# Kernel optimization log

Hardware: AMD Instinct MI355X
Metric: run time of the kernel (lower is better)

Reference implementation:

```python
import jax, jax.numpy as jnp
import numpy as np
from jax import lax

UNITS1 = 256  # lstm_layer (second LSTM, return_sequences=False)
UNITS2 = 256  # hidden_lstm (first LSTM, return_sequences=True)
FEAT = 128


def _glorot(key, shape):
    fan_in, fan_out = shape[0], shape[1]
    lim = jnp.sqrt(6.0 / (fan_in + fan_out))
    return jax.random.uniform(key, shape, jnp.float32, -lim, lim)


def setup_inputs() -> dict:
    key = jax.random.key(0)
    ks = jax.random.split(key, 9)
    B, T = 128, 1024
    x = jax.random.normal(ks[0], (B, T, FEAT), jnp.float32)
    # Layer 1 (hidden_lstm): Keras kernel [in, 4H], recurrent_kernel [H, 4H], bias [4H]
    W1 = _glorot(ks[1], (FEAT, 4 * UNITS2))
    U1 = _glorot(ks[2], (UNITS2, 4 * UNITS2))
    b1 = jnp.zeros((4 * UNITS2,), jnp.float32).at[UNITS2:2 * UNITS2].set(1.0)  # Keras unit_forget_bias
    # Layer 2 (lstm_layer)
    W2 = _glorot(ks[3], (UNITS2, 4 * UNITS1))
    U2 = _glorot(ks[4], (UNITS1, 4 * UNITS1))
    b2 = jnp.zeros((4 * UNITS1,), jnp.float32).at[UNITS1:2 * UNITS1].set(1.0)
    # Output dense: 1 unit, relu
    Wd = _glorot(ks[5], (UNITS1, 1))
    bd = jnp.zeros((1,), jnp.float32)
    return {"x": x, "W1": W1, "U1": U1, "b1": b1,
            "W2": W2, "U2": U2, "b2": b2, "Wd": Wd, "bd": bd}


def _lstm(x, W, U, b, return_sequences):
    # x: [B, T, F]; Keras gate order i, f, c(candidate), o.
    B = x.shape[0]
    H = U.shape[0]
    xW = jnp.einsum('btf,fg->btg', x, W) + b  # precompute input projections: [B, T, 4H]

    def step(carry, xw_t):
        h, c = carry
        g = xw_t + h @ U  # [B, 4H]
        i, f, cand, o = jnp.split(g, 4, axis=-1)
        i = jax.nn.sigmoid(i)
        f = jax.nn.sigmoid(f)
        cand = jnp.tanh(cand)
        o = jax.nn.sigmoid(o)
        c = f * c + i * cand
        h = o * jnp.tanh(c)
        return (h, c), h

    init = (jnp.zeros((B, H), x.dtype), jnp.zeros((B, H), x.dtype))
    (h_last, _), hs = lax.scan(step, init, jnp.swapaxes(xW, 0, 1))  # hs: [T, B, H]
    return jnp.swapaxes(hs, 0, 1) if return_sequences else h_last


def reference(x, W1, U1, b1, W2, U2, b2, Wd, bd):
    h_seq = _lstm(x, W1, U1, b1, return_sequences=True)   # hidden_lstm: [B, T, U2]
    h_last = _lstm(h_seq, W2, U2, b2, return_sequences=False)  # lstm_layer: [B, U1]
    return jax.nn.relu(h_last @ Wd + bd)  # [B, 1]
```

## Files before the change

### kernel.cpp

```cpp
#include <hip/hip_runtime.h>

typedef __bf16 bf16x8 __attribute__((ext_vector_type(8)));
typedef float  f32x4  __attribute__((ext_vector_type(4)));
typedef unsigned short u16;
typedef unsigned int   u32;
typedef unsigned long long u64;

#define NB 128
#define NT 1024
#define NF 128
#define NH 256
#define NG 1024
#define M_ROWS (NB*NT)

__device__ __forceinline__ u16 f2bf(float f) {
  union { float f; u32 u; } c; c.f = f;
  u32 u = c.u;
  return (u16)((u + 0x7fffu + ((u >> 16) & 1u)) >> 16);
}

__device__ __forceinline__ float sigm(float x) { return 1.f / (1.f + __expf(-x)); }
__device__ __forceinline__ float tanh_(float x) { return 1.f - 2.f / (1.f + __expf(2.f * x)); }

__device__ __forceinline__ f32x4 mm(bf16x8 a, bf16x8 b, f32x4 c) {
  return __builtin_amdgcn_mfma_f32_16x16x32_bf16(a, b, c, 0, 0, 0);
}

__device__ __forceinline__ u64 a_ld64(const u64* p) {
  return __hip_atomic_load((u64*)p, __ATOMIC_RELAXED, __HIP_MEMORY_SCOPE_AGENT);
}
__device__ __forceinline__ void a_st64(u64* p, u64 v) {
  __hip_atomic_store(p, v, __ATOMIC_RELAXED, __HIP_MEMORY_SCOPE_AGENT);
}
__device__ __forceinline__ void vm0() { asm volatile("s_waitcnt vmcnt(0)" ::: "memory"); }

__device__ __forceinline__ bool poll_ge(u32* c, u32 target, long& budget) {
  while (__hip_atomic_load(c, __ATOMIC_RELAXED, __HIP_MEMORY_SCOPE_AGENT) < target) {
    if (--budget <= 0) return false;
  }
  asm volatile("" ::: "memory");
  return true;
}

__global__ void prep(u32* __restrict__ flags) {
  if (blockIdx.x == 0 && threadIdx.x < 256) flags[threadIdx.x] = 0;
}

template<bool L1>
__device__ __forceinline__ void scan(
    const float* __restrict__ U, const float* __restrict__ W,
    const float* __restrict__ bias, const float* __restrict__ xf,
    u64* hseq, u64* h2, u32* cnt1, u32* cnt2, float* hlast,
    int g, int j, float (*gl)[16][68])
{
  const int tid  = threadIdx.x;
  const int lane = tid & 63;
  const int w    = tid >> 6;
  const int l15  = lane & 15, l16 = lane >> 4;
  constexpr int KIN  = L1 ? NF : NH;
  constexpr int KTIN = KIN / 32;

  const int colb = w * NH + j * 64;

  bf16x8 wfr[KTIN][4];
#pragma unroll
  for (int kt = 0; kt < KTIN; ++kt) {
    const int k0 = kt * 32 + l16 * 8;
#pragma unroll
    for (int nt = 0; nt < 4; ++nt) {
      const float* wp = W + (long)k0 * NG + colb + nt * 16 + l15;
      union { u16 s[8]; bf16x8 v; } cv;
#pragma unroll
      for (int e = 0; e < 8; ++e) cv.s[e] = f2bf(wp[(long)e * NG]);
      wfr[kt][nt] = cv.v;
    }
  }
  bf16x8 ufr[8][4];
#pragma unroll
  for (int kt = 0; kt < 8; ++kt) {
    const int k0 = kt * 32 + l16 * 8;
#pragma unroll
    for (int nt = 0; nt < 4; ++nt) {
      const float* up = U + (long)k0 * NG + colb + nt * 16 + l15;
      union { u16 s[8]; bf16x8 v; } cv;
#pragma unroll
      for (int e = 0; e < 8; ++e) cv.s[e] = f2bf(up[(long)e * NG]);
      ufr[kt][nt] = cv.v;
    }
  }

  const int prow = tid & 15;
  const int ublk = tid >> 4;
  const int b    = g * 16 + prow;
  const int ucol = j * 64 + ublk * 4;

  float bv[4][4];
#pragma unroll
  for (int gg = 0; gg < 4; ++gg)
#pragma unroll
    for (int q = 0; q < 4; ++q) bv[gg][q] = bias[gg * NH + ucol + q];

  u32* c1 = cnt1 + g * 16;
  u32* c2 = cnt2 + g * 16;
  const long abatch = (long)(g * 16 + l15) * NT;

  float cst[4] = {0.f, 0.f, 0.f, 0.f};
  long budget = 20000000;
  bool dead = false;

  for (int t = 0; t < NT; ++t) {
    bf16x8 ax[KTIN];
    if constexpr (L1) {
      const float* xp0 = xf + (abatch + t) * NF;
      f32x4 xraw[KTIN][2];
#pragma unroll
      for (int kt = 0; kt < KTIN; ++kt) {
        const float* xp = xp0 + kt * 32 + l16 * 8;
        xraw[kt][0] = *reinterpret_cast<const f32x4*>(xp);
        xraw[kt][1] = *reinterpret_cast<const f32x4*>(xp + 4);
      }
#pragma unroll
      for (int kt = 0; kt < KTIN; ++kt) {
        union { u16 s[8]; bf16x8 v; } cv;
#pragma unroll
        for (int e = 0; e < 4; ++e) {
          cv.s[e] = f2bf(xraw[kt][0][e]); cv.s[4 + e] = f2bf(xraw[kt][1][e]);
        }
        ax[kt] = cv.v;
      }
    } else {
      if (!dead && !poll_ge(c1, 16u * (u32)(t + 1), budget)) dead = true;
      u64* xb = hseq + (abatch + t) * 64;
#pragma unroll
      for (int kt = 0; kt < KTIN; ++kt) {
        union { u64 q[2]; bf16x8 v; } cv;
        cv.q[0] = a_ld64(xb + kt * 8 + l16 * 2);
        cv.q[1] = a_ld64(xb + kt * 8 + l16 * 2 + 1);
        ax[kt] = cv.v;
      }
    }

    f32x4 acc[4] = {};
#pragma unroll
    for (int kt = 0; kt < KTIN; ++kt)
#pragma unroll
      for (int nt = 0; nt < 4; ++nt) acc[nt] = mm(ax[kt], wfr[kt][nt], acc[nt]);

    if (t > 0) {
      u32* cr = L1 ? c1 : c2;
      if (!dead && !poll_ge(cr, 16u * (u32)t, budget)) dead = true;
      u64* hb;
      if constexpr (L1) hb = hseq + (abatch + (t - 1)) * 64;
      else              hb = h2 + ((((long)((t + 1) & 1) * 8 + g) * 16) + l15) * 64;
      bf16x8 af[8];
#pragma unroll
      for (int kt = 0; kt < 8; ++kt) {
        union { u64 q[2]; bf16x8 v; } cv;
        cv.q[0] = a_ld64(hb + kt * 8 + l16 * 2);
        cv.q[1] = a_ld64(hb + kt * 8 + l16 * 2 + 1);
        af[kt] = cv.v;
      }
#pragma unroll
      for (int kt = 0; kt < 8; ++kt)
#pragma unroll
        for (int nt = 0; nt < 4; ++nt) acc[nt] = mm(af[kt], ufr[kt][nt], acc[nt]);
    }

#pragma unroll
    for (int nt = 0; nt < 4; ++nt)
#pragma unroll
      for (int r = 0; r < 4; ++r)
        gl[w][l16 * 4 + r][nt * 16 + l15] = acc[nt][r];
    __syncthreads();

    f32x4 gi = *reinterpret_cast<const f32x4*>(&gl[0][prow][ublk * 4]);
    f32x4 gf = *reinterpret_cast<const f32x4*>(&gl[1][prow][ublk * 4]);
    f32x4 gc = *reinterpret_cast<const f32x4*>(&gl[2][prow][ublk * 4]);
    f32x4 go = *reinterpret_cast<const f32x4*>(&gl[3][prow][ublk * 4]);
    __syncthreads();
    float hh[4];
#pragma unroll
    for (int q = 0; q < 4; ++q) {
      float iv = sigm(gi[q] + bv[0][q]);
      float fv = sigm(gf[q] + bv[1][q]);
      float cd = tanh_(gc[q] + bv[2][q]);
      float ov = sigm(go[q] + bv[3][q]);
      cst[q] = fv * cst[q] + iv * cd;
      hh[q] = ov * tanh_(cst[q]);
    }
    union { u16 s[4]; u64 q; } hp;
#pragma unroll
    for (int q = 0; q < 4; ++q) hp.s[q] = f2bf(hh[q]);

    if constexpr (L1) {
      a_st64(hseq + ((long)b * NT + t) * 64 + (ucol >> 2), hp.q);
    } else {
      a_st64(h2 + ((((long)(t & 1) * 8 + g) * 16) + prow) * 64 + (ucol >> 2), hp.q);
      if (t == NT - 1)
        *reinterpret_cast<f32x4*>(hlast + (long)b * NH + ucol) =
            f32x4{hh[0], hh[1], hh[2], hh[3]};
    }

    vm0();
    if (lane == 0)
      __hip_atomic_fetch_add(L1 ? c1 : c2, 1u, __ATOMIC_RELAXED, __HIP_MEMORY_SCOPE_AGENT);
  }
}

__global__ __launch_bounds__(256, 1) void lstm_fused(
    const float* __restrict__ x,
    const float* __restrict__ W1, const float* __restrict__ U1, const float* __restrict__ b1,
    const float* __restrict__ W2, const float* __restrict__ U2, const float* __restrict__ b2,
    u64* hseq, u64* h2, u32* flags, float* hlast)
{
  __shared__ __align__(16) float gl[4][16][68];
  const int bid = blockIdx.x;
  const int sb  = bid & 31;
  u32* cnt1 = flags;
  u32* cnt2 = flags + 128;
  if (bid < 32)
    scan<true >(U1, W1, b1, x, hseq, nullptr, cnt1, cnt2, nullptr, sb & 7, sb >> 3, gl);
  else
    scan<false>(U2, W2, b2, nullptr, hseq, h2, cnt1, cnt2, hlast, sb & 7, sb >> 3, gl);
}

__global__ void dense_out(const float* __restrict__ hl, const float* __restrict__ Wd,
                          const float* __restrict__ bd, float* __restrict__ out) {
  int b = blockIdx.x, l = threadIdx.x;
  f32x4 h  = *reinterpret_cast<const f32x4*>(hl + (long)b * NH + l * 4);
  f32x4 wv = *reinterpret_cast<const f32x4*>(Wd + l * 4);
  float s = h[0] * wv[0] + h[1] * wv[1] + h[2] * wv[2] + h[3] * wv[3];
#pragma unroll
  for (int off = 32; off > 0; off >>= 1) s += __shfl_down(s, off);
  if (l == 0) out[b] = fmaxf(s + bd[0], 0.f);
}

extern "C" void kernel_launch(void* const* d_in, const int* in_sizes, int n_in,
                              void* d_out, int out_size, void* d_ws, size_t ws_size,
                              hipStream_t stream) {
  const float* x  = (const float*)d_in[0];
  const float* W1 = (const float*)d_in[1];
  const float* U1 = (const float*)d_in[2];
  const float* b1 = (const float*)d_in[3];
  const float* W2 = (const float*)d_in[4];
  const float* U2 = (const float*)d_in[5];
  const float* b2 = (const float*)d_in[6];
  const float* Wd = (const float*)d_in[7];
  const float* bd = (const float*)d_in[8];
  float* out = (float*)d_out;

  char* ws = (char*)d_ws;
  size_t off = 0;
  auto alloc = [&](size_t bytes) -> char* {
    char* p = ws + off;
    off = (off + bytes + 255) & ~(size_t)255;
    return p;
  };
  u64*   hseq  = (u64*)  alloc((size_t)M_ROWS * NH * 2);
  u64*   h2    = (u64*)  alloc((size_t)2 * 8 * 16 * NH * 2);
  float* hlast = (float*)alloc((size_t)NB * NH * 4);
  u32*   flags = (u32*)  alloc(1024);

  if (off > ws_size) {
    hipMemsetAsync(d_out, 0x42, (size_t)out_size * sizeof(float), stream);
    return;
  }

  prep<<<1, 256, 0, stream>>>(flags);
  lstm_fused<<<64, 256, 0, stream>>>(x, W1, U1, b1, W2, U2, b2, hseq, h2, flags, hlast);
  dense_out<<<128, 64, 0, stream>>>(hlast, Wd, bd, out);
}
```

Before: 5.936 ms.

## Use per-block step tags and XCC-local sc0 loads when groups share an XCD

```diff
diff --git a/kernel.cpp b/kernel.cpp
--- a/kernel.cpp
+++ b/kernel.cpp
@@ -13,29 +13,67 @@
 #define NG 1024
 #define M_ROWS (NB*NT)
 
+#define TAGS1_OFF 0
+#define TAGS2_OFF 512
+#define PING_OFF  1024
+#define META_OFF  1536
+#define RDY_OFF   1600
+#define DONE_OFF  1664
+#define ABRT_OFF  1696
+#define FLAGS_N   2048
+
 __device__ __forceinline__ u16 f2bf(float f) {
   union { float f; u32 u; } c; c.f = f;
   u32 u = c.u;
   return (u16)((u + 0x7fffu + ((u >> 16) & 1u)) >> 16);
 }
-
 __device__ __forceinline__ float sigm(float x) { return 1.f / (1.f + __expf(-x)); }
 __device__ __forceinline__ float tanh_(float x) { return 1.f - 2.f / (1.f + __expf(2.f * x)); }
-
 __device__ __forceinline__ f32x4 mm(bf16x8 a, bf16x8 b, f32x4 c) {
   return __builtin_amdgcn_mfma_f32_16x16x32_bf16(a, b, c, 0, 0, 0);
 }
-
-__device__ __forceinline__ u64 a_ld64(const u64* p) {
-  return __hip_atomic_load((u64*)p, __ATOMIC_RELAXED, __HIP_MEMORY_SCOPE_AGENT);
-}
-__device__ __forceinline__ void a_st64(u64* p, u64 v) {
-  __hip_atomic_store(p, v, __ATOMIC_RELAXED, __HIP_MEMORY_SCOPE_AGENT);
-}
 __device__ __forceinline__ void vm0() { asm volatile("s_waitcnt vmcnt(0)" ::: "memory"); }
-
-__device__ __forceinline__ bool poll_ge(u32* c, u32 target, long& budget) {
-  while (__hip_atomic_load(c, __ATOMIC_RELAXED, __HIP_MEMORY_SCOPE_AGENT) < target) {
+__device__ __forceinline__ void sb0() { __builtin_amdgcn_sched_barrier(0); }
+
+__device__ __forceinline__ u32 a_ld32(const u32* p) { return __hip_atomic_load((u32*)p, __ATOMIC_RELAXED, __HIP_MEMORY_SCOPE_AGENT); }
+__device__ __forceinline__ u64 a_ld64(const u64* p) { return __hip_atomic_load((u64*)p, __ATOMIC_RELAXED, __HIP_MEMORY_SCOPE_AGENT); }
+__device__ __forceinline__ void a_st32(u32* p, u32 v) { __hip_atomic_store(p, v, __ATOMIC_RELAXED, __HIP_MEMORY_SCOPE_AGENT); }
+__device__ __forceinline__ void a_st64(u64* p, u64 v) { __hip_atomic_store(p, v, __ATOMIC_RELAXED, __HIP_MEMORY_SCOPE_AGENT); }
+__device__ __forceinline__ void a_add32(u32* p, u32 v) { __hip_atomic_fetch_add(p, v, __ATOMIC_RELAXED, __HIP_MEMORY_SCOPE_AGENT); }
+
+__device__ __forceinline__ u64 s_ld64(const u64* p) {
+  u64 r; asm volatile("global_load_dwordx2 %0, %1, off sc0" : "=v"(r) : "v"(p) : "memory"); return r;
+}
+__device__ __forceinline__ u32 s_ld32w(const u32* p) {
+  u32 r; asm volatile("global_load_dword %0, %1, off sc0\n\ts_waitcnt vmcnt(0)" : "=v"(r) : "v"(p) : "memory"); return r;
+}
+__device__ __forceinline__ void s_st64(u64* p, u64 v) {
+  asm volatile("global_store_dwordx2 %0, %1, off sc0" :: "v"(p), "v"(v) : "memory");
+}
+__device__ __forceinline__ void s_st32(u32* p, u32 v) {
+  asm volatile("global_store_dword %0, %1, off sc0" :: "v"(p), "v"(v) : "memory");
+}
+
+template<bool FAST> __device__ __forceinline__ u64 dld64(const u64* p) {
+  if constexpr (FAST) return s_ld64(p); else return a_ld64(p);
+}
+template<bool FAST> __device__ __forceinline__ void dwait() {
+  if constexpr (FAST) { vm0(); sb0(); }
+}
+template<bool FAST> __device__ __forceinline__ void dst64(u64* p, u64 v) {
+  if constexpr (FAST) s_st64(p, v); else a_st64(p, v);
+}
+template<bool FAST> __device__ __forceinline__ void tst32(u32* p, u32 v) {
+  if constexpr (FAST) s_st32(p, v); else a_st32(p, v);
+}
+template<bool FAST> __device__ __forceinline__ bool poll4(const u32* tg, u32 target, long& budget) {
+  const u64* p = (const u64*)tg;
+  for (;;) {
+    u64 a, b;
+    if constexpr (FAST) { a = s_ld64(p); b = s_ld64(p + 1); vm0(); sb0(); }
+    else                { a = a_ld64(p); b = a_ld64(p + 1); }
+    if ((u32)a >= target && (u32)(a >> 32) >= target &&
+        (u32)b >= target && (u32)(b >> 32) >= target) break;
     if (--budget <= 0) return false;
   }
   asm volatile("" ::: "memory");
@@ -43,23 +81,20 @@
 }
 
 __global__ void prep(u32* __restrict__ flags) {
-  if (blockIdx.x == 0 && threadIdx.x < 256) flags[threadIdx.x] = 0;
-}
-
-template<bool L1>
-__device__ __forceinline__ void scan(
-    const float* __restrict__ U, const float* __restrict__ W,
-    const float* __restrict__ bias, const float* __restrict__ xf,
-    u64* hseq, u64* h2, u32* cnt1, u32* cnt2, float* hlast,
-    int g, int j, float (*gl)[16][68])
+  int i = blockIdx.x * 256 + threadIdx.x;
+  if (i < FLAGS_N) flags[i] = 0;
+}
+
+template<bool IS1, bool FAST>
+__device__ void scan(const float* __restrict__ U, const float* __restrict__ W,
+                     const float* __restrict__ bias, const float* __restrict__ xf,
+                     u64* hseq, u64* h2, u32* flags, float* hlast,
+                     int g, int j, float (*gl)[16][68])
 {
-  const int tid  = threadIdx.x;
-  const int lane = tid & 63;
-  const int w    = tid >> 6;
-  const int l15  = lane & 15, l16 = lane >> 4;
-  constexpr int KIN  = L1 ? NF : NH;
+  const int tid = threadIdx.x, lane = tid & 63, w = tid >> 6;
+  const int l15 = lane & 15, l16 = lane >> 4;
+  constexpr int KIN  = IS1 ? NF : NH;
   constexpr int KTIN = KIN / 32;
-
   const int colb = w * NH + j * 64;
 
   bf16x8 wfr[KTIN][4];
@@ -89,10 +124,8 @@
     }
   }
 
-  const int prow = tid & 15;
-  const int ublk = tid >> 4;
-  const int b    = g * 16 + prow;
-  const int ucol = j * 64 + ublk * 4;
+  const int prow = tid & 15, ublk = tid >> 4;
+  const int b = g * 16 + prow, ucol = j * 64 + ublk * 4;
 
   float bv[4][4];
 #pragma unroll
@@ -100,17 +133,18 @@
 #pragma unroll
     for (int q = 0; q < 4; ++q) bv[gg][q] = bias[gg * NH + ucol + q];
 
-  u32* c1 = cnt1 + g * 16;
-  u32* c2 = cnt2 + g * 16;
+  u32* t1 = flags + TAGS1_OFF + g * 64;
+  u32* t2 = flags + TAGS2_OFF + g * 64;
+  u32* mytag = (IS1 ? t1 : t2) + j;
   const long abatch = (long)(g * 16 + l15) * NT;
 
   float cst[4] = {0.f, 0.f, 0.f, 0.f};
-  long budget = 20000000;
+  long budget = 1000000;
   bool dead = false;
 
   for (int t = 0; t < NT; ++t) {
     bf16x8 ax[KTIN];
-    if constexpr (L1) {
+    if constexpr (IS1) {
       const float* xp0 = xf + (abatch + t) * NF;
       f32x4 xraw[KTIN][2];
 #pragma unroll
@@ -129,13 +163,19 @@
         ax[kt] = cv.v;
       }
     } else {
-      if (!dead && !poll_ge(c1, 16u * (u32)(t + 1), budget)) dead = true;
+      if (!dead && !poll4<FAST>(t1, (u32)(t + 1), budget)) dead = true;
       u64* xb = hseq + (abatch + t) * 64;
+      u64 xr[KTIN][2];
+#pragma unroll
+      for (int kt = 0; kt < KTIN; ++kt) {
+        xr[kt][0] = dld64<FAST>(xb + kt * 8 + l16 * 2);
+        xr[kt][1] = dld64<FAST>(xb + kt * 8 + l16 * 2 + 1);
+      }
+      dwait<FAST>();
 #pragma unroll
       for (int kt = 0; kt < KTIN; ++kt) {
         union { u64 q[2]; bf16x8 v; } cv;
-        cv.q[0] = a_ld64(xb + kt * 8 + l16 * 2);
-        cv.q[1] = a_ld64(xb + kt * 8 + l16 * 2 + 1);
+        cv.q[0] = xr[kt][0]; cv.q[1] = xr[kt][1];
         ax[kt] = cv.v;
       }
     }
@@ -147,23 +187,24 @@
       for (int nt = 0; nt < 4; ++nt) acc[nt] = mm(ax[kt], wfr[kt][nt], acc[nt]);
 
     if (t > 0) {
-      u32* cr = L1 ? c1 : c2;
-      if (!dead && !poll_ge(cr, 16u * (u32)t, budget)) dead = true;
-      u64* hb;
-      if constexpr (L1) hb = hseq + (abatch + (t - 1)) * 64;
-      else              hb = h2 + ((((long)((t + 1) & 1) * 8 + g) * 16) + l15) * 64;
-      bf16x8 af[8];
+      if (!dead && !poll4<FAST>(IS1 ? t1 : t2, (u32)t, budget)) dead = true;
+      const u64* hb;
+      if constexpr (IS1) hb = hseq + (abatch + (t - 1)) * 64;
+      else               hb = h2 + ((((long)((t + 1) & 1) * 8 + g) * 16) + l15) * 64;
+      u64 hr[8][2];
+#pragma unroll
+      for (int kt = 0; kt < 8; ++kt) {
+        hr[kt][0] = dld64<FAST>(hb + kt * 8 + l16 * 2);
+        hr[kt][1] = dld64<FAST>(hb + kt * 8 + l16 * 2 + 1);
+      }
+      dwait<FAST>();
 #pragma unroll
       for (int kt = 0; kt < 8; ++kt) {
         union { u64 q[2]; bf16x8 v; } cv;
-        cv.q[0] = a_ld64(hb + kt * 8 + l16 * 2);
-        cv.q[1] = a_ld64(hb + kt * 8 + l16 * 2 + 1);
-        af[kt] = cv.v;
-      }
-#pragma unroll
-      for (int kt = 0; kt < 8; ++kt)
-#pragma unroll
-        for (int nt = 0; nt < 4; ++nt) acc[nt] = mm(af[kt], ufr[kt][nt], acc[nt]);
+        cv.q[0] = hr[kt][0]; cv.q[1] = hr[kt][1];
+#pragma unroll
+        for (int nt = 0; nt < 4; ++nt) acc[nt] = mm(cv.v, ufr[kt][nt], acc[nt]);
+      }
     }
 
 #pragma unroll
@@ -177,7 +218,6 @@
     f32x4 gf = *reinterpret_cast<const f32x4*>(&gl[1][prow][ublk * 4]);
     f32x4 gc = *reinterpret_cast<const f32x4*>(&gl[2][prow][ublk * 4]);
     f32x4 go = *reinterpret_cast<const f32x4*>(&gl[3][prow][ublk * 4]);
-    __syncthreads();
     float hh[4];
 #pragma unroll
     for (int q = 0; q < 4; ++q) {
@@ -192,18 +232,18 @@
 #pragma unroll
     for (int q = 0; q < 4; ++q) hp.s[q] = f2bf(hh[q]);
 
-    if constexpr (L1) {
-      a_st64(hseq + ((long)b * NT + t) * 64 + (ucol >> 2), hp.q);
+    if constexpr (IS1) {
+      dst64<FAST>(hseq + ((long)b * NT + t) * 64 + (ucol >> 2), hp.q);
     } else {
-      a_st64(h2 + ((((long)(t & 1) * 8 + g) * 16) + prow) * 64 + (ucol >> 2), hp.q);
+      dst64<FAST>(h2 + ((((long)(t & 1) * 8 + g) * 16) + prow) * 64 + (ucol >> 2), hp.q);
       if (t == NT - 1)
         *reinterpret_cast<f32x4*>(hlast + (long)b * NH + ucol) =
             f32x4{hh[0], hh[1], hh[2], hh[3]};
     }
 
     vm0();
-    if (lane == 0)
-      __hip_atomic_fetch_add(L1 ? c1 : c2, 1u, __ATOMIC_RELAXED, __HIP_MEMORY_SCOPE_AGENT);
+    __syncthreads();
+    if (tid == 0) tst32<FAST>(mytag, (u32)(t + 1));
   }
 }
 
@@ -214,14 +254,70 @@
     u64* hseq, u64* h2, u32* flags, float* hlast)
 {
   __shared__ __align__(16) float gl[4][16][68];
-  const int bid = blockIdx.x;
-  const int sb  = bid & 31;
-  u32* cnt1 = flags;
-  u32* cnt2 = flags + 128;
-  if (bid < 32)
-    scan<true >(U1, W1, b1, x, hseq, nullptr, cnt1, cnt2, nullptr, sb & 7, sb >> 3, gl);
-  else
-    scan<false>(U2, W2, b2, nullptr, hseq, h2, cnt1, cnt2, hlast, sb & 7, sb >> 3, gl);
+  __shared__ int sm;
+  const int bid = blockIdx.x, tid = threadIdx.x, lane = tid & 63;
+  const int sb = bid & 31, g = sb & 7, j = sb >> 3;
+  const bool is1 = bid < 32;
+
+  u32* meta = flags + META_OFF;
+  u32* rdy  = flags + RDY_OFF;
+  u32* ping = flags + PING_OFF;
+  u32* done = flags + DONE_OFF;
+  u32* abrt = flags + ABRT_OFF;
+
+  u32 xcc = 0;
+  asm volatile("s_getreg_b32 %0, hwreg(HW_REG_XCC_ID)" : "=s"(xcc));
+  if (tid == 0) { a_st32(meta + bid, xcc + 1u); vm0(); a_add32(rdy, 1u); }
+  bool ok = true;
+  { long hb = 2000000;
+    while (a_ld32(rdy) < 64u) { if (--hb <= 0) { ok = false; break; } } }
+  asm volatile("" ::: "memory");
+  u32 mv = 0; if (ok) mv = a_ld32(meta + lane);
+  u32 m0 = __shfl(mv, 0);
+  const bool alldeg = __all(mv == m0);
+  u32 v0 = __shfl(mv, g);
+  bool co = ok && !alldeg && (v0 != 0);
+#pragma unroll
+  for (int k = 1; k < 8; ++k) co = co && (__shfl(mv, g + 8 * k) == v0);
+
+  if (tid == 0) {
+    bool fail = !co;
+    if (co) {
+      const int r = is1 ? j : (4 + j);
+      u32* slot = ping + g * 64 + r;
+      u32* prev = ping + g * 64 + ((r + 7) & 7);
+      for (u32 k = 1; k <= 3u && !fail; ++k) {
+        if (r == 0) {
+          s_st32(slot, k);
+          long pb = 20000;
+          while (s_ld32w(prev) < k) { if (--pb <= 0) { fail = true; break; } }
+        } else {
+          long pb = 20000;
+          while (s_ld32w(prev) < k) { if (--pb <= 0) { fail = true; break; } }
+          if (!fail) s_st32(slot, k);
+        }
+      }
+      vm0();
+    }
+    if (fail) a_st32(abrt + g, 1u);
+    vm0();
+    a_add32(done + g, 1u);
+    long db = 2000000; bool jok = true;
+    while (a_ld32(done + g) < 8u) { if (--db <= 0) { jok = false; break; } }
+    asm volatile("" ::: "memory");
+    u32 ab = a_ld32(abrt + g);
+    sm = (jok && ab == 0u) ? 1 : 0;
+  }
+  __syncthreads();
+  const bool fast = (sm == 1);
+
+  if (is1) {
+    if (fast) scan<true,  true >(U1, W1, b1, x, hseq, h2, flags, hlast, g, j, gl);
+    else      scan<true,  false>(U1, W1, b1, x, hseq, h2, flags, hlast, g, j, gl);
+  } else {
+    if (fast) scan<false, true >(U2, W2, b2, nullptr, hseq, h2, flags, hlast, g, j, gl);
+    else      scan<false, false>(U2, W2, b2, nullptr, hseq, h2, flags, hlast, g, j, gl);
+  }
 }
 
 __global__ void dense_out(const float* __restrict__ hl, const float* __restrict__ Wd,
@@ -259,14 +355,14 @@
   u64*   hseq  = (u64*)  alloc((size_t)M_ROWS * NH * 2);
   u64*   h2    = (u64*)  alloc((size_t)2 * 8 * 16 * NH * 2);
   float* hlast = (float*)alloc((size_t)NB * NH * 4);
-  u32*   flags = (u32*)  alloc(1024);
+  u32*   flags = (u32*)  alloc(FLAGS_N * 4);
 
   if (off > ws_size) {
     hipMemsetAsync(d_out, 0x42, (size_t)out_size * sizeof(float), stream);
     return;
   }
 
-  prep<<<1, 256, 0, stream>>>(flags);
+  prep<<<8, 256, 0, stream>>>(flags);
   lstm_fused<<<64, 256, 0, stream>>>(x, W1, U1, b1, W2, U2, b2, hseq, h2, flags, hlast);
   dense_out<<<128, 64, 0, stream>>>(hlast, Wd, bd, out);
 }
```

New measurement: 7.876 ms. +32.7%, slower.

## Poll step counters from one thread with sleep and batch recurrent loads

Applied to the files above, without the earlier changes.

```diff
diff --git a/kernel.cpp b/kernel.cpp
--- a/kernel.cpp
+++ b/kernel.cpp
@@ -18,48 +18,32 @@
   u32 u = c.u;
   return (u16)((u + 0x7fffu + ((u >> 16) & 1u)) >> 16);
 }
-
 __device__ __forceinline__ float sigm(float x) { return 1.f / (1.f + __expf(-x)); }
 __device__ __forceinline__ float tanh_(float x) { return 1.f - 2.f / (1.f + __expf(2.f * x)); }
-
 __device__ __forceinline__ f32x4 mm(bf16x8 a, bf16x8 b, f32x4 c) {
   return __builtin_amdgcn_mfma_f32_16x16x32_bf16(a, b, c, 0, 0, 0);
 }
-
-__device__ __forceinline__ u64 a_ld64(const u64* p) {
-  return __hip_atomic_load((u64*)p, __ATOMIC_RELAXED, __HIP_MEMORY_SCOPE_AGENT);
-}
-__device__ __forceinline__ void a_st64(u64* p, u64 v) {
-  __hip_atomic_store(p, v, __ATOMIC_RELAXED, __HIP_MEMORY_SCOPE_AGENT);
-}
 __device__ __forceinline__ void vm0() { asm volatile("s_waitcnt vmcnt(0)" ::: "memory"); }
 
-__device__ __forceinline__ bool poll_ge(u32* c, u32 target, long& budget) {
-  while (__hip_atomic_load(c, __ATOMIC_RELAXED, __HIP_MEMORY_SCOPE_AGENT) < target) {
-    if (--budget <= 0) return false;
-  }
-  asm volatile("" ::: "memory");
-  return true;
-}
+__device__ __forceinline__ u32 a_ld32(const u32* p) { return __hip_atomic_load((u32*)p, __ATOMIC_RELAXED, __HIP_MEMORY_SCOPE_AGENT); }
+__device__ __forceinline__ u64 a_ld64(const u64* p) { return __hip_atomic_load((u64*)p, __ATOMIC_RELAXED, __HIP_MEMORY_SCOPE_AGENT); }
+__device__ __forceinline__ void a_st64(u64* p, u64 v) { __hip_atomic_store(p, v, __ATOMIC_RELAXED, __HIP_MEMORY_SCOPE_AGENT); }
+__device__ __forceinline__ void a_add32(u32* p, u32 v) { __hip_atomic_fetch_add(p, v, __ATOMIC_RELAXED, __HIP_MEMORY_SCOPE_AGENT); }
 
 __global__ void prep(u32* __restrict__ flags) {
   if (blockIdx.x == 0 && threadIdx.x < 256) flags[threadIdx.x] = 0;
 }
 
-template<bool L1>
-__device__ __forceinline__ void scan(
-    const float* __restrict__ U, const float* __restrict__ W,
-    const float* __restrict__ bias, const float* __restrict__ xf,
-    u64* hseq, u64* h2, u32* cnt1, u32* cnt2, float* hlast,
-    int g, int j, float (*gl)[16][68])
+template<bool IS1>
+__device__ void scan(const float* __restrict__ U, const float* __restrict__ W,
+                     const float* __restrict__ bias, const float* __restrict__ xf,
+                     u64* hseq, u64* h2, u32* c1, u32* c2, float* hlast,
+                     int g, int j, float (*gl)[16][68])
 {
-  const int tid  = threadIdx.x;
-  const int lane = tid & 63;
-  const int w    = tid >> 6;
-  const int l15  = lane & 15, l16 = lane >> 4;
-  constexpr int KIN  = L1 ? NF : NH;
+  const int tid = threadIdx.x, lane = tid & 63, w = tid >> 6;
+  const int l15 = lane & 15, l16 = lane >> 4;
+  constexpr int KIN  = IS1 ? NF : NH;
   constexpr int KTIN = KIN / 32;
-
   const int colb = w * NH + j * 64;
 
   bf16x8 wfr[KTIN][4];
@@ -89,10 +73,8 @@
     }
   }
 
-  const int prow = tid & 15;
-  const int ublk = tid >> 4;
-  const int b    = g * 16 + prow;
-  const int ucol = j * 64 + ublk * 4;
+  const int prow = tid & 15, ublk = tid >> 4;
+  const int b = g * 16 + prow, ucol = j * 64 + ublk * 4;
 
   float bv[4][4];
 #pragma unroll
@@ -100,17 +82,16 @@
 #pragma unroll
     for (int q = 0; q < 4; ++q) bv[gg][q] = bias[gg * NH + ucol + q];
 
-  u32* c1 = cnt1 + g * 16;
-  u32* c2 = cnt2 + g * 16;
   const long abatch = (long)(g * 16 + l15) * NT;
 
   float cst[4] = {0.f, 0.f, 0.f, 0.f};
-  long budget = 20000000;
+  long budget = 2000000;
   bool dead = false;
 
   for (int t = 0; t < NT; ++t) {
     bf16x8 ax[KTIN];
-    if constexpr (L1) {
+
+    if constexpr (IS1) {
       const float* xp0 = xf + (abatch + t) * NF;
       f32x4 xraw[KTIN][2];
 #pragma unroll
@@ -128,56 +109,105 @@
         }
         ax[kt] = cv.v;
       }
+      f32x4 acc[4] = {};
+#pragma unroll
+      for (int kt = 0; kt < KTIN; ++kt)
+#pragma unroll
+        for (int nt = 0; nt < 4; ++nt) acc[nt] = mm(ax[kt], wfr[kt][nt], acc[nt]);
+
+      if (t > 0) {
+        if (tid == 0 && !dead) {
+          const u32 tgt = 16u * (u32)t;
+          while (a_ld32(c1) < tgt) {
+            __builtin_amdgcn_s_sleep(1);
+            if (--budget <= 0) { dead = true; break; }
+          }
+        }
+        __syncthreads();
+        asm volatile("" ::: "memory");
+        const u64* hb = hseq + (abatch + (t - 1)) * 64;
+        u64 hr[8][2];
+#pragma unroll
+        for (int kt = 0; kt < 8; ++kt) {
+          hr[kt][0] = a_ld64(hb + kt * 8 + l16 * 2);
+          hr[kt][1] = a_ld64(hb + kt * 8 + l16 * 2 + 1);
+        }
+#pragma unroll
+        for (int kt = 0; kt < 8; ++kt) {
+          union { u64 q[2]; bf16x8 v; } cv;
+          cv.q[0] = hr[kt][0]; cv.q[1] = hr[kt][1];
+#pragma unroll
+          for (int nt = 0; nt < 4; ++nt) acc[nt] = mm(cv.v, ufr[kt][nt], acc[nt]);
+        }
+      }
+#pragma unroll
+      for (int nt = 0; nt < 4; ++nt)
+#pragma unroll
+        for (int r = 0; r < 4; ++r)
+          gl[w][l16 * 4 + r][nt * 16 + l15] = acc[nt][r];
     } else {
-      if (!dead && !poll_ge(c1, 16u * (u32)(t + 1), budget)) dead = true;
-      u64* xb = hseq + (abatch + t) * 64;
+      if (tid == 0 && !dead) {
+        const u32 tgtF = 16u * (u32)(t + 1);
+        const u32 tgtR = 16u * (u32)t;
+        for (;;) {
+          u32 v1 = a_ld32(c1);
+          u32 v2 = (t > 0) ? a_ld32(c2) : tgtR;
+          if (v1 >= tgtF && v2 >= tgtR) break;
+          __builtin_amdgcn_s_sleep(1);
+          if (--budget <= 0) { dead = true; break; }
+        }
+      }
+      __syncthreads();
+      asm volatile("" ::: "memory");
+
+      const u64* xb = hseq + (abatch + t) * 64;
+      u64 xr[KTIN][2];
+#pragma unroll
+      for (int kt = 0; kt < KTIN; ++kt) {
+        xr[kt][0] = a_ld64(xb + kt * 8 + l16 * 2);
+        xr[kt][1] = a_ld64(xb + kt * 8 + l16 * 2 + 1);
+      }
+      u64 hr[8][2];
+      if (t > 0) {
+        const u64* hb = h2 + ((((long)((t + 1) & 1) * 8 + g) * 16) + l15) * 64;
+#pragma unroll
+        for (int kt = 0; kt < 8; ++kt) {
+          hr[kt][0] = a_ld64(hb + kt * 8 + l16 * 2);
+          hr[kt][1] = a_ld64(hb + kt * 8 + l16 * 2 + 1);
+        }
+      }
 #pragma unroll
       for (int kt = 0; kt < KTIN; ++kt) {
         union { u64 q[2]; bf16x8 v; } cv;
-        cv.q[0] = a_ld64(xb + kt * 8 + l16 * 2);
-        cv.q[1] = a_ld64(xb + kt * 8 + l16 * 2 + 1);
+        cv.q[0] = xr[kt][0]; cv.q[1] = xr[kt][1];
         ax[kt] = cv.v;
       }
-    }
-
-    f32x4 acc[4] = {};
-#pragma unroll
-    for (int kt = 0; kt < KTIN; ++kt)
-#pragma unroll
-      for (int nt = 0; nt < 4; ++nt) acc[nt] = mm(ax[kt], wfr[kt][nt], acc[nt]);
-
-    if (t > 0) {
-      u32* cr = L1 ? c1 : c2;
-      if (!dead && !poll_ge(cr, 16u * (u32)t, budget)) dead = true;
-      u64* hb;
-      if constexpr (L1) hb = hseq + (abatch + (t - 1)) * 64;
-      else              hb = h2 + ((((long)((t + 1) & 1) * 8 + g) * 16) + l15) * 64;
-      bf16x8 af[8];
-#pragma unroll
-      for (int kt = 0; kt < 8; ++kt) {
-        union { u64 q[2]; bf16x8 v; } cv;
-        cv.q[0] = a_ld64(hb + kt * 8 + l16 * 2);
-        cv.q[1] = a_ld64(hb + kt * 8 + l16 * 2 + 1);
-        af[kt] = cv.v;
-      }
-#pragma unroll
-      for (int kt = 0; kt < 8; ++kt)
-#pragma unroll
-        for (int nt = 0; nt < 4; ++nt) acc[nt] = mm(af[kt], ufr[kt][nt], acc[nt]);
-    }
-
-#pragma unroll
-    for (int nt = 0; nt < 4; ++nt)
-#pragma unroll
-      for (int r = 0; r < 4; ++r)
-        gl[w][l16 * 4 + r][nt * 16 + l15] = acc[nt][r];
+      f32x4 acc[4] = {};
+#pragma unroll
+      for (int kt = 0; kt < KTIN; ++kt)
+#pragma unroll
+        for (int nt = 0; nt < 4; ++nt) acc[nt] = mm(ax[kt], wfr[kt][nt], acc[nt]);
+      if (t > 0) {
+#pragma unroll
+        for (int kt = 0; kt < 8; ++kt) {
+          union { u64 q[2]; bf16x8 v; } cv;
+          cv.q[0] = hr[kt][0]; cv.q[1] = hr[kt][1];
+#pragma unroll
+          for (int nt = 0; nt < 4; ++nt) acc[nt] = mm(cv.v, ufr[kt][nt], acc[nt]);
+        }
+      }
+#pragma unroll
+      for (int nt = 0; nt < 4; ++nt)
+#pragma unroll
+        for (int r = 0; r < 4; ++r)
+          gl[w][l16 * 4 + r][nt * 16 + l15] = acc[nt][r];
+    }
+
     __syncthreads();
-
     f32x4 gi = *reinterpret_cast<const f32x4*>(&gl[0][prow][ublk * 4]);
     f32x4 gf = *reinterpret_cast<const f32x4*>(&gl[1][prow][ublk * 4]);
     f32x4 gc = *reinterpret_cast<const f32x4*>(&gl[2][prow][ublk * 4]);
     f32x4 go = *reinterpret_cast<const f32x4*>(&gl[3][prow][ublk * 4]);
-    __syncthreads();
     float hh[4];
 #pragma unroll
     for (int q = 0; q < 4; ++q) {
@@ -192,7 +222,7 @@
 #pragma unroll
     for (int q = 0; q < 4; ++q) hp.s[q] = f2bf(hh[q]);
 
-    if constexpr (L1) {
+    if constexpr (IS1) {
       a_st64(hseq + ((long)b * NT + t) * 64 + (ucol >> 2), hp.q);
     } else {
       a_st64(h2 + ((((long)(t & 1) * 8 + g) * 16) + prow) * 64 + (ucol >> 2), hp.q);
@@ -200,10 +230,8 @@
         *reinterpret_cast<f32x4*>(hlast + (long)b * NH + ucol) =
             f32x4{hh[0], hh[1], hh[2], hh[3]};
     }
-
     vm0();
-    if (lane == 0)
-      __hip_atomic_fetch_add(L1 ? c1 : c2, 1u, __ATOMIC_RELAXED, __HIP_MEMORY_SCOPE_AGENT);
+    if (lane == 0) a_add32(IS1 ? c1 : c2, 1u);
   }
 }
 
@@ -215,13 +243,13 @@
 {
   __shared__ __align__(16) float gl[4][16][68];
   const int bid = blockIdx.x;
-  const int sb  = bid & 31;
-  u32* cnt1 = flags;
-  u32* cnt2 = flags + 128;
+  const int sb  = bid & 31, g = sb & 7, j = sb >> 3;
+  u32* c1 = flags + g * 16;
+  u32* c2 = flags + 128 + g * 16;
   if (bid < 32)
-    scan<true >(U1, W1, b1, x, hseq, nullptr, cnt1, cnt2, nullptr, sb & 7, sb >> 3, gl);
+    scan<true >(U1, W1, b1, x, hseq, h2, c1, c2, nullptr, g, j, gl);
   else
-    scan<false>(U2, W2, b2, nullptr, hseq, h2, cnt1, cnt2, hlast, sb & 7, sb >> 3, gl);
+    scan<false>(U2, W2, b2, nullptr, hseq, h2, c1, c2, hlast, g, j, gl);
 }
 
 __global__ void dense_out(const float* __restrict__ hl, const float* __restrict__ Wd,
```

Result: slower. 6.278 ms (+5.8%).
